# Performance work log

Hardware: AMD Instinct MI355X
Metric: run time of the kernel (lower is better)

Reference implementation:

```python
import jax, jax.numpy as jnp
import numpy as np

B = 1024      # number of subgraphs in the batch
S = 128       # nodes per subgraph (last node is the anchor)
N = B * S     # total nodes
E = 2_097_152 # total edges (avg degree 16)
F_IN = 300
F_OUT = 64


def setup_inputs() -> dict:
    key = jax.random.key(0)
    kx, kg, ks, kd, kw = jax.random.split(key, 5)
    in_feat = jax.random.normal(kx, (N, F_IN), dtype=jnp.float32)
    # edges constrained within subgraphs (batched DGL graph semantics)
    gid = jax.random.randint(kg, (E,), 0, B)
    src = (gid * S + jax.random.randint(ks, (E,), 0, S)).astype(jnp.int32)
    dst = (gid * S + jax.random.randint(kd, (E,), 0, S)).astype(jnp.int32)
    W = jax.random.normal(kw, (F_IN, F_OUT), dtype=jnp.float32) * 0.05
    b = jnp.zeros((F_OUT,), dtype=jnp.float32)
    prelu_a = jnp.float32(0.25)  # nn.PReLU default single parameter
    return {"in_feat": in_feat, "W": W, "b": b, "prelu_a": prelu_a,
            "src": src, "dst": dst}


def reference(in_feat, W, b, prelu_a, src, dst):
    ones = jnp.ones((E,), dtype=jnp.float32)
    deg_out = jnp.clip(jax.ops.segment_sum(ones, src, num_segments=N), 1.0)
    deg_in = jnp.clip(jax.ops.segment_sum(ones, dst, num_segments=N), 1.0)
    # GraphConv norm='both': weight first (in_feats > out_feats), then SpMM
    x = in_feat * jax.lax.rsqrt(deg_out)[:, None]
    h = x @ W                                   # [N, F_OUT]
    agg = jax.ops.segment_sum(h[src], dst, num_segments=N)
    h = agg * jax.lax.rsqrt(deg_in)[:, None] + b
    # PReLU
    h = jnp.where(h > 0, h, prelu_a * h)
    # ragged per-subgraph mean over all nodes except the last (anchor)
    node_idx = jnp.arange(N)
    seg = node_idx // S                          # subgraph id per node
    not_anchor = ((node_idx % S) != (S - 1)).astype(h.dtype)
    pool_sum = jax.ops.segment_sum(h * not_anchor[:, None], seg, num_segments=B)
    subgraph_pool_emb = pool_sum / jnp.float32(S - 1)
    anchor_out = h[(jnp.arange(B) + 1) * S - 1]  # last node of each subgraph
    return subgraph_pool_emb, anchor_out
```

## Files before the change

### kernel.cpp

```cpp
#include <hip/hip_runtime.h>
#include <hip/hip_bf16.h>

#define NNODES 131072
#define NEDGES 2097152
#define BSUB   1024
#define SSUB   128
#define FIN    300
#define FOUT   64
#define NCHUNK 256
#define CHEDGE 8192

typedef __attribute__((ext_vector_type(8))) short short8;
typedef __attribute__((ext_vector_type(8))) unsigned short ushort8;
typedef __attribute__((ext_vector_type(4))) float f32x4;

__device__ inline unsigned short f2bfbits(float f) {
    union { __hip_bfloat16 h; unsigned short u; } cv;
    cv.h = __float2bfloat16(f);
    return cv.u;
}
__device__ inline float bf2f(unsigned short b) {
    return __uint_as_float(((unsigned)b) << 16);
}

__global__ __launch_bounds__(256) void prep_w_kernel(const float* __restrict__ W,
                                                     short* __restrict__ wfrag,
                                                     int* __restrict__ gcnt) {
    int idx = blockIdx.x * 256 + threadIdx.x;
    if (idx < BSUB) gcnt[idx] = 0;
    if (idx >= 2560) return;
    int ct   = idx / 640;
    int rem  = idx % 640;
    int kt   = rem / 64;
    int lane = rem % 64;
    int col  = ct * 16 + (lane & 15);
    int kb   = kt * 32 + (lane >> 4) * 8;
#pragma unroll
    for (int e = 0; e < 8; ++e) {
        int k = kb + e;
        float v = (k < FIN) ? W[(size_t)k * FOUT + col] : 0.f;
        wfrag[(size_t)idx * 8 + e] = (short)f2bfbits(v);
    }
}

__global__ __launch_bounds__(256) void bucket_kernel(const int* __restrict__ src,
                                                     const int* __restrict__ dst,
                                                     int* __restrict__ gcnt,
                                                     unsigned short* __restrict__ bkt) {
    __shared__ unsigned short epack[CHEDGE];
    __shared__ unsigned short eg[CHEDGE];
    __shared__ int hist[BSUB];
    const int t = threadIdx.x;
    for (int i = t; i < BSUB; i += 256) hist[i] = 0;
    __syncthreads();
    const int4* sp = (const int4*)(src + (size_t)blockIdx.x * CHEDGE);
    const int4* dp = (const int4*)(dst + (size_t)blockIdx.x * CHEDGE);
    for (int i = t; i < CHEDGE / 4; i += 256) {
        int4 s4 = sp[i], d4 = dp[i];
#pragma unroll
        for (int k = 0; k < 4; ++k) {
            int s = (k == 0) ? s4.x : (k == 1) ? s4.y : (k == 2) ? s4.z : s4.w;
            int d = (k == 0) ? d4.x : (k == 1) ? d4.y : (k == 2) ? d4.z : d4.w;
            int g = s >> 7;
            epack[i * 4 + k] = (unsigned short)(((s & 127) << 7) | (d & 127));
            eg[i * 4 + k] = (unsigned short)g;
            atomicAdd(&hist[g], 1);
        }
    }
    __syncthreads();
    for (int i = t; i < BSUB; i += 256) {
        int c = hist[i];
        hist[i] = c ? atomicAdd(&gcnt[i], c) : 0;
    }
    __syncthreads();
    for (int i = t; i < CHEDGE; i += 256) {
        int g = eg[i];
        int r = atomicAdd(&hist[g], 1);
        bkt[((size_t)g << 12) + r] = epack[i];
    }
}

__global__ __launch_bounds__(256) void gemm_kernel(const float* __restrict__ x,
                                                   const short* __restrict__ wfrag,
                                                   unsigned short* __restrict__ hb) {
    const int wave = threadIdx.x >> 6;
    const int lane = threadIdx.x & 63;
    const int rowbase = (blockIdx.x * 4 + wave) * 16;
    const int arow = rowbase + (lane & 15);
    const int kgrp = lane >> 4;

    f32x4 acc[4];
#pragma unroll
    for (int c = 0; c < 4; ++c) acc[c] = (f32x4){0.f, 0.f, 0.f, 0.f};

    const float* ap = x + (size_t)arow * FIN + kgrp * 8;
#pragma unroll
    for (int kt = 0; kt < 9; ++kt) {
        f32x4 lo = *(const f32x4*)(ap + kt * 32);
        f32x4 hi = *(const f32x4*)(ap + kt * 32 + 4);
        short8 afr;
        afr[0] = (short)f2bfbits(lo[0]); afr[1] = (short)f2bfbits(lo[1]);
        afr[2] = (short)f2bfbits(lo[2]); afr[3] = (short)f2bfbits(lo[3]);
        afr[4] = (short)f2bfbits(hi[0]); afr[5] = (short)f2bfbits(hi[1]);
        afr[6] = (short)f2bfbits(hi[2]); afr[7] = (short)f2bfbits(hi[3]);
#pragma unroll
        for (int ct = 0; ct < 4; ++ct) {
            short8 bfr = *(const short8*)(wfrag + ((size_t)(ct * 10 + kt) * 64 + lane) * 8);
            acc[ct] = __builtin_amdgcn_mfma_f32_16x16x32_bf16(afr, bfr, acc[ct], 0, 0, 0);
        }
    }
    {
        short8 afr;
#pragma unroll
        for (int e = 0; e < 8; ++e) {
            int k = 288 + kgrp * 8 + e;
            float v = (k < FIN) ? x[(size_t)arow * FIN + k] : 0.f;
            afr[e] = (short)f2bfbits(v);
        }
#pragma unroll
        for (int ct = 0; ct < 4; ++ct) {
            short8 bfr = *(const short8*)(wfrag + ((size_t)(ct * 10 + 9) * 64 + lane) * 8);
            acc[ct] = __builtin_amdgcn_mfma_f32_16x16x32_bf16(afr, bfr, acc[ct], 0, 0, 0);
        }
    }
    const int orow = rowbase + (lane >> 4) * 4;
    const int colb = lane & 15;
#pragma unroll
    for (int ct = 0; ct < 4; ++ct)
#pragma unroll
        for (int r = 0; r < 4; ++r)
            hb[(size_t)(orow + r) * FOUT + ct * 16 + colb] = f2bfbits(acc[ct][r]);
}

__global__ __launch_bounds__(256) void agg_pool_kernel(const unsigned short* __restrict__ hb,
                                                       const unsigned short* __restrict__ bkt,
                                                       const int* __restrict__ gcnt,
                                                       const float* __restrict__ bias,
                                                       const float* __restrict__ prelu,
                                                       float* __restrict__ out) {
    __shared__ unsigned short hl[SSUB][FOUT];
    __shared__ unsigned char  es[SSUB][64];
    __shared__ int   din[SSUB];
    __shared__ int   dout[SSUB];
    __shared__ float rout[SSUB];
    __shared__ float ps[4][FOUT];

    const int g = blockIdx.x;
    const int t = threadIdx.x;
    const int lane = t & 63;
    const int w = t >> 6;

    {
        const ushort8* hsrc = (const ushort8*)(hb + (size_t)g * SSUB * FOUT);
        ushort8* hdst = (ushort8*)&hl[0][0];
        for (int i = t; i < 1024; i += 256) hdst[i] = hsrc[i];
    }
    if (t < SSUB) { din[t] = 0; dout[t] = 0; }
    __syncthreads();

    const int cnt = gcnt[g];
    const unsigned short* eb = bkt + ((size_t)g << 12);

    for (int i = t; i < cnt; i += 256) {
        unsigned e = eb[i];
        int s = e >> 7, d = e & 127;
        int r = atomicAdd(&din[d], 1);
        es[d][r & 63] = (unsigned char)s;
        atomicAdd(&dout[s], 1);
    }
    __syncthreads();
    if (t < SSUB) rout[t] = rsqrtf((float)max(dout[t], 1));
    __syncthreads();

    const float bv = bias[lane];
    const float a = prelu[0];
    float pool = 0.f;
#pragma unroll 4
    for (int ii = 0; ii < 32; ++ii) {
        int d = w + 4 * ii;
        int cd = min(din[d], 64);
        float accv = 0.f;
        const unsigned* ew = (const unsigned*)&es[d][0];
        int nw = (cd + 3) >> 2;
        for (int p = 0; p < nw; ++p) {
            unsigned wd = ew[p];
            int rem = cd - p * 4;
#pragma unroll
            for (int b = 0; b < 4; ++b) {
                if (b < rem) {
                    int s = (wd >> (8 * b)) & 127;
                    accv += bf2f(hl[s][lane]) * rout[s];
                }
            }
        }
        float v = accv * rsqrtf((float)max(din[d], 1)) + bv;
        v = (v > 0.f) ? v : a * v;
        if (d == SSUB - 1)
            out[(size_t)(BSUB + g) * FOUT + lane] = v;
        else
            pool += v;
    }
    ps[w][lane] = pool;
    __syncthreads();
    if (w == 0) {
        float s = (ps[0][lane] + ps[1][lane]) + (ps[2][lane] + ps[3][lane]);
        out[(size_t)g * FOUT + lane] = s * (1.0f / 127.0f);
    }
}

extern "C" void kernel_launch(void* const* d_in, const int* in_sizes, int n_in,
                              void* d_out, int out_size, void* d_ws, size_t ws_size,
                              hipStream_t stream) {
    const float* in_feat = (const float*)d_in[0];
    const float* W       = (const float*)d_in[1];
    const float* bias    = (const float*)d_in[2];
    const float* prelu   = (const float*)d_in[3];
    const int*   src     = (const int*)d_in[4];
    const int*   dst     = (const int*)d_in[5];
    float* out = (float*)d_out;

    char* ws = (char*)d_ws;
    int*            gcnt  = (int*)(ws);
    short*          wfrag = (short*)(ws + 65536);
    unsigned short* bkt   = (unsigned short*)(ws + (1u << 20));
    unsigned short* hb    = (unsigned short*)(ws + (16u << 20));

    hipLaunchKernelGGL(prep_w_kernel,   dim3(10),        dim3(256), 0, stream, W, wfrag, gcnt);
    hipLaunchKernelGGL(bucket_kernel,   dim3(NCHUNK),    dim3(256), 0, stream, src, dst, gcnt, bkt);
    hipLaunchKernelGGL(gemm_kernel,     dim3(NNODES/64), dim3(256), 0, stream, in_feat, wfrag, hb);
    hipLaunchKernelGGL(agg_pool_kernel, dim3(BSUB),      dim3(256), 0, stream, hb, bkt, gcnt, bias, prelu, out);
}
```

Baseline: 121.0 us.

## Merge edge bucketing and GEMM into one launch and drop bucket LDS staging

Merges the edge-bucketing kernel and the bf16 MFMA projection GEMM into one grid, with the first 256 blocks doing bucketing and the rest doing GEMM. The two independent stages can then overlap on the GPU and one launch boundary goes away. The bucketing path no longer stages packed edges in shared memory. It builds the histogram from src alone, then rereads src and dst from global memory to scatter, trading extra global reads for smaller LDS use and better occupancy.

```diff
diff --git a/kernel.cpp b/kernel.cpp
--- a/kernel.cpp
+++ b/kernel.cpp
@@ -43,49 +43,50 @@
     }
 }
 
-__global__ __launch_bounds__(256) void bucket_kernel(const int* __restrict__ src,
-                                                     const int* __restrict__ dst,
-                                                     int* __restrict__ gcnt,
-                                                     unsigned short* __restrict__ bkt) {
-    __shared__ unsigned short epack[CHEDGE];
-    __shared__ unsigned short eg[CHEDGE];
-    __shared__ int hist[BSUB];
-    const int t = threadIdx.x;
-    for (int i = t; i < BSUB; i += 256) hist[i] = 0;
-    __syncthreads();
-    const int4* sp = (const int4*)(src + (size_t)blockIdx.x * CHEDGE);
-    const int4* dp = (const int4*)(dst + (size_t)blockIdx.x * CHEDGE);
-    for (int i = t; i < CHEDGE / 4; i += 256) {
-        int4 s4 = sp[i], d4 = dp[i];
-#pragma unroll
-        for (int k = 0; k < 4; ++k) {
-            int s = (k == 0) ? s4.x : (k == 1) ? s4.y : (k == 2) ? s4.z : s4.w;
-            int d = (k == 0) ? d4.x : (k == 1) ? d4.y : (k == 2) ? d4.z : d4.w;
-            int g = s >> 7;
-            epack[i * 4 + k] = (unsigned short)(((s & 127) << 7) | (d & 127));
-            eg[i * 4 + k] = (unsigned short)g;
-            atomicAdd(&hist[g], 1);
-        }
-    }
-    __syncthreads();
-    for (int i = t; i < BSUB; i += 256) {
-        int c = hist[i];
-        hist[i] = c ? atomicAdd(&gcnt[i], c) : 0;
-    }
-    __syncthreads();
-    for (int i = t; i < CHEDGE; i += 256) {
-        int g = eg[i];
-        int r = atomicAdd(&hist[g], 1);
-        bkt[((size_t)g << 12) + r] = epack[i];
-    }
-}
-
-__global__ __launch_bounds__(256) void gemm_kernel(const float* __restrict__ x,
-                                                   const short* __restrict__ wfrag,
-                                                   unsigned short* __restrict__ hb) {
+__global__ __launch_bounds__(256) void bucket_gemm_kernel(const int* __restrict__ src,
+                                                          const int* __restrict__ dst,
+                                                          int* __restrict__ gcnt,
+                                                          unsigned short* __restrict__ bkt,
+                                                          const float* __restrict__ x,
+                                                          const short* __restrict__ wfrag,
+                                                          unsigned short* __restrict__ hb) {
+    if (blockIdx.x < NCHUNK) {
+        __shared__ int hist[BSUB];
+        const int cb = blockIdx.x;
+        const int t = threadIdx.x;
+        for (int i = t; i < BSUB; i += 256) hist[i] = 0;
+        __syncthreads();
+        const int4* sp = (const int4*)(src + (size_t)cb * CHEDGE);
+        for (int i = t; i < CHEDGE / 4; i += 256) {
+            int4 v = sp[i];
+            atomicAdd(&hist[v.x >> 7], 1);
+            atomicAdd(&hist[v.y >> 7], 1);
+            atomicAdd(&hist[v.z >> 7], 1);
+            atomicAdd(&hist[v.w >> 7], 1);
+        }
+        __syncthreads();
+        for (int i = t; i < BSUB; i += 256) {
+            int c = hist[i];
+            hist[i] = c ? atomicAdd(&gcnt[i], c) : 0;
+        }
+        __syncthreads();
+        const int4* dp = (const int4*)(dst + (size_t)cb * CHEDGE);
+        for (int i = t; i < CHEDGE / 4; i += 256) {
+            int4 s4 = sp[i], d4 = dp[i];
+#pragma unroll
+            for (int k = 0; k < 4; ++k) {
+                int s = (k == 0) ? s4.x : (k == 1) ? s4.y : (k == 2) ? s4.z : s4.w;
+                int d = (k == 0) ? d4.x : (k == 1) ? d4.y : (k == 2) ? d4.z : d4.w;
+                int g = s >> 7;
+                int r = atomicAdd(&hist[g], 1);
+                bkt[((size_t)g << 12) + r] = (unsigned short)(((s & 127) << 7) | (d & 127));
+            }
+        }
+        return;
+    }
     const int wave = threadIdx.x >> 6;
     const int lane = threadIdx.x & 63;
-    const int rowbase = (blockIdx.x * 4 + wave) * 16;
+    const int rowbase = ((blockIdx.x - NCHUNK) * 4 + wave) * 16;
     const int arow = rowbase + (lane & 15);
     const int kgrp = lane >> 4;
 
@@ -225,8 +226,8 @@
     unsigned short* bkt   = (unsigned short*)(ws + (1u << 20));
     unsigned short* hb    = (unsigned short*)(ws + (16u << 20));
 
-    hipLaunchKernelGGL(prep_w_kernel,   dim3(10),        dim3(256), 0, stream, W, wfrag, gcnt);
-    hipLaunchKernelGGL(bucket_kernel,   dim3(NCHUNK),    dim3(256), 0, stream, src, dst, gcnt, bkt);
-    hipLaunchKernelGGL(gemm_kernel,     dim3(NNODES/64), dim3(256), 0, stream, in_feat, wfrag, hb);
-    hipLaunchKernelGGL(agg_pool_kernel, dim3(BSUB),      dim3(256), 0, stream, hb, bkt, gcnt, bias, prelu, out);
-}
+    hipLaunchKernelGGL(prep_w_kernel,     dim3(10),                 dim3(256), 0, stream, W, wfrag, gcnt);
+    hipLaunchKernelGGL(bucket_gemm_kernel,dim3(NCHUNK + NNODES/64), dim3(256), 0, stream,
+                       src, dst, gcnt, bkt, in_feat, wfrag, hb);
+    hipLaunchKernelGGL(agg_pool_kernel,   dim3(BSUB),               dim3(256), 0, stream, hb, bkt, gcnt, bias, prelu, out);
+}
```

Result: no change. 120.9 us (-0.1%).
